# Kernel tuning notes

Measured on AMD Instinct MI355X. Metric: run time of the kernel, lower is better.

## Reference

```python
import jax, jax.numpy as jnp
import numpy as np

L, H, C, V, T_MAX = 12, 12, 768, 50257, 1024
D = C // H
LN_EPS = 1e-5


def layer_norm(x, w, b):
    m = jnp.mean(x, axis=-1, keepdims=True)
    v = jnp.mean(jnp.square(x - m), axis=-1, keepdims=True)
    return (x - m) * jax.lax.rsqrt(v + LN_EPS) * w + b


def setup_inputs() -> dict:
    key = jax.random.key(0)
    ks = jax.random.split(key, 16)
    B, T = 2, 1024
    s = 0.02
    inp = {
        "idx": jax.random.randint(ks[0], (B, T), 0, V),
        "wte": jax.random.normal(ks[1], (V, C), jnp.float32) * s,
        "wpe": jax.random.normal(ks[2], (T_MAX, C), jnp.float32) * s,
        # stacked per-layer params, leading axis = layer
        "ln1_w": jnp.ones((L, C), jnp.float32),
        "ln1_b": jnp.zeros((L, C), jnp.float32),
        "Wq": jax.random.normal(ks[3], (L, C, C), jnp.float32) * s,
        "bq": jnp.zeros((L, C), jnp.float32),
        "Wk": jax.random.normal(ks[4], (L, C, C), jnp.float32) * s,
        "bk": jnp.zeros((L, C), jnp.float32),
        "Wv": jax.random.normal(ks[5], (L, C, C), jnp.float32) * s,
        "bv": jnp.zeros((L, C), jnp.float32),
        "Wo": jax.random.normal(ks[6], (L, C, C), jnp.float32) * (s / np.sqrt(2 * L)),
        "bo": jnp.zeros((L, C), jnp.float32),
        "ln2_w": jnp.ones((L, C), jnp.float32),
        "ln2_b": jnp.zeros((L, C), jnp.float32),
        "Wfc": jax.random.normal(ks[7], (L, C, 4 * C), jnp.float32) * s,
        "bfc": jnp.zeros((L, 4 * C), jnp.float32),
        "Wpr": jax.random.normal(ks[8], (L, 4 * C, C), jnp.float32) * (s / np.sqrt(2 * L)),
        "bpr": jnp.zeros((L, C), jnp.float32),
        "ln_f_w": jnp.ones((C,), jnp.float32),
        "ln_f_b": jnp.zeros((C,), jnp.float32),
        "Wlm": jax.random.normal(ks[9], (C, V), jnp.float32) * s,
    }
    return inp


def _forward(idx, wte, wpe, ln1_w, ln1_b, Wq, bq, Wk, bk, Wv, bv, Wo, bo,
             ln2_w, ln2_b, Wfc, bfc, Wpr, bpr, ln_f_w, ln_f_b, Wlm):
    B, T = idx.shape
    x = wte[idx] + wpe[jnp.arange(T)][None, :, :]  # (B,T,C)
    causal = jnp.tril(jnp.ones((T, T), bool))  # (T,T) causal mask
    scale = 1.0 / np.sqrt(D)
    neg_inf = jnp.finfo(x.dtype).min

    def block(x, p):
        (l1w, l1b, wq, bq_, wk, bk_, wv, bv_, wo, bo_,
         l2w, l2b, wfc, bfc_, wpr, bpr_) = p
        h = layer_norm(x, l1w, l1b)
        q = (h @ wq + bq_).reshape(B, T, H, D)
        k = (h @ wk + bk_).reshape(B, T, H, D)
        v = (h @ wv + bv_).reshape(B, T, H, D)
        scores = jnp.einsum("bqhd,bkhd->bhqk", q, k) * scale
        scores = jnp.where(causal[None, None], scores, neg_inf)
        attn = jax.nn.softmax(scores, axis=-1)
        y = jnp.einsum("bhqk,bkhd->bqhd", attn, v).reshape(B, T, C)
        x = x + y @ wo + bo_
        h2 = layer_norm(x, l2w, l2b)
        x = x + jax.nn.gelu(h2 @ wfc + bfc_, approximate=False) @ wpr + bpr_
        return x, None

    params = (ln1_w, ln1_b, Wq, bq, Wk, bk, Wv, bv, Wo, bo,
              ln2_w, ln2_b, Wfc, bfc, Wpr, bpr)
    x, _ = jax.lax.scan(block, x, params)
    x = layer_norm(x, ln_f_w, ln_f_b)
    logits = x @ Wlm  # (B,T,V)
    return logits


def reference(idx, wte, wpe, ln1_w, ln1_b, Wq, bq, Wk, bk, Wv, bv, Wo, bo,
              ln2_w, ln2_b, Wfc, bfc, Wpr, bpr, ln_f_w, ln_f_b, Wlm):
    return _forward(idx, wte, wpe, ln1_w, ln1_b, Wq, bq, Wk, bk, Wv, bv, Wo, bo,
                    ln2_w, ln2_b, Wfc, bfc, Wpr, bpr, ln_f_w, ln_f_b, Wlm)
```

## Files before the change

### kernel.cpp

```cpp
#include <hip/hip_runtime.h>
#include <math.h>
#include <cstddef>


#define Cdim 768
#define Hn   12
#define Ln   12
#define Tn   1024
#define Bn   2
#define Mrows (Bn * Tn)

typedef unsigned short ushort_t;
typedef __bf16 bf16x8 __attribute__((ext_vector_type(8)));
typedef float  f32x4  __attribute__((ext_vector_type(4)));

__device__ __forceinline__ ushort_t f2bf(float v) {
    union { float f; unsigned int u; } x; x.f = v;
    unsigned int r = x.u + 0x7fffu + ((x.u >> 16) & 1u);
    return (ushort_t)(r >> 16);
}
__device__ __forceinline__ float gelu_f(float v) {
    return 0.5f * v * (1.0f + erff(v * 0.70710678118654752f));
}
__device__ __forceinline__ void gload16(const void* g, void* l) {
    __builtin_amdgcn_global_load_lds(
        (const __attribute__((address_space(1))) unsigned int*)g,
        (__attribute__((address_space(3))) unsigned int*)l, 16, 0, 0);
}

__global__ void embed_k(const int* __restrict__ idx, const float* __restrict__ wte,
                        const float* __restrict__ wpe, float* __restrict__ x) {
    int i = blockIdx.x * 256 + threadIdx.x;
    int c  = i % Cdim;
    int bt = i / Cdim;
    int t  = bt % Tn;
    int tok = idx[bt];
    x[i] = wte[(size_t)tok * Cdim + c] + wpe[(size_t)t * Cdim + c];
}

__global__ __launch_bounds__(256) void ln_k(const float* __restrict__ x,
                                            const float* __restrict__ w,
                                            const float* __restrict__ b,
                                            ushort_t* __restrict__ out) {
    int row = blockIdx.x;
    const float* xr = x + (size_t)row * Cdim;
    int t = threadIdx.x;
    float v0 = xr[t], v1 = xr[t + 256], v2 = xr[t + 512];
    float s = v0 + v1 + v2;
    #pragma unroll
    for (int o = 32; o > 0; o >>= 1) s += __shfl_xor(s, o);
    __shared__ float red[8];
    int wid = t >> 6;
    if ((t & 63) == 0) red[wid] = s;
    __syncthreads();
    float mean = (red[0] + red[1] + red[2] + red[3]) * (1.0f / 768.0f);
    float d0 = v0 - mean, d1 = v1 - mean, d2 = v2 - mean;
    float sq = d0 * d0 + d1 * d1 + d2 * d2;
    #pragma unroll
    for (int o = 32; o > 0; o >>= 1) sq += __shfl_xor(sq, o);
    if ((t & 63) == 0) red[4 + wid] = sq;
    __syncthreads();
    float var = (red[4] + red[5] + red[6] + red[7]) * (1.0f / 768.0f);
    float rstd = rsqrtf(var + 1e-5f);
    ushort_t* orow = out + (size_t)row * Cdim;
    orow[t]       = f2bf(d0 * rstd * w[t]       + b[t]);
    orow[t + 256] = f2bf(d1 * rstd * w[t + 256] + b[t + 256]);
    orow[t + 512] = f2bf(d2 * rstd * w[t + 512] + b[t + 512]);
}

__device__ __forceinline__ void tconv_tile(const float* __restrict__ W,
                                           ushort_t* __restrict__ WT,
                                           int K, int N, int n0, int k0, bool guard) {
    __shared__ float t[32][33];
    int x = threadIdx.x & 31, y = threadIdx.x >> 5;
    #pragma unroll
    for (int j = 0; j < 4; ++j) {
        int kk = k0 + y + j * 8, nn = n0 + x;
        t[y + j * 8][x] = (!guard || nn < N) ? W[(size_t)kk * N + nn] : 0.0f;
    }
    __syncthreads();
    #pragma unroll
    for (int j = 0; j < 4; ++j) {
        int nn = n0 + y + j * 8, kk = k0 + x;
        WT[(size_t)nn * K + kk] = f2bf(t[x][y + j * 8]);
    }
}

__global__ __launch_bounds__(256) void wconv_k(const float* __restrict__ W,
                                               ushort_t* __restrict__ WT,
                                               int K, int N) {
    tconv_tile(W, WT, K, N, blockIdx.x * 32, blockIdx.y * 32, true);
}

__global__ __launch_bounds__(256) void conv_layer_k(
    const float* __restrict__ Wq, const float* __restrict__ Wk,
    const float* __restrict__ Wv, const float* __restrict__ Wo,
    const float* __restrict__ Wfc, const float* __restrict__ Wpr,
    const float* __restrict__ bq, const float* __restrict__ bk,
    const float* __restrict__ bv,
    ushort_t* __restrict__ wqkvt, ushort_t* __restrict__ wot,
    ushort_t* __restrict__ wfct,  ushort_t* __restrict__ wprt,
    float* __restrict__ bqkv) {
    int bid = blockIdx.x;
    if (bid < 2304) {
        int z = bid / 576, t = bid % 576;
        const float* W = (z == 0) ? Wq : (z == 1) ? Wk : (z == 2) ? Wv : Wo;
        ushort_t* dst = (z < 3) ? (wqkvt + (size_t)z * 768 * 768) : wot;
        tconv_tile(W, dst, 768, 768, (t % 24) * 32, (t / 24) * 32, false);
    } else if (bid < 4608) {
        int t = bid - 2304;
        tconv_tile(Wfc, wfct, 768, 3072, (t % 96) * 32, (t / 96) * 32, false);
    } else if (bid < 6912) {
        int t = bid - 4608;
        tconv_tile(Wpr, wprt, 3072, 768, (t % 24) * 32, (t / 24) * 32, false);
    } else {
        int i = (bid - 6912) * 256 + threadIdx.x;
        bqkv[i] = (i < 768) ? bq[i] : (i < 1536 ? bk[i - 768] : bv[i - 1536]);
    }
}

template <int BM, int BN, int TH, int WGN, bool BIAS, bool GELU_, bool OUTBF16, bool XCD>
__global__ __launch_bounds__(TH, 2) void gemm_pipe_k(
    const ushort_t* __restrict__ A,
    const ushort_t* __restrict__ Bt,
    const float* __restrict__ bias,
    void* __restrict__ Cout,
    int M, int N, int K, int cpx, int mtiles) {
    constexpr int SA = BM * 128;
    constexpr int SB = BN * 128;
    constexpr int WM = BM / 2;
    constexpr int WN = BN / WGN;
    constexpr int FM = WM / 16;
    constexpr int FN = WN / 16;
    constexpr int RJ = TH / 8;
    __shared__ char lds[2 * (SA + SB)];
    char* Abase = lds;
    char* Bbase = lds + 2 * SA;

    const int tid = threadIdx.x;
    const int lane = tid & 63;
    const int w = tid >> 6;
    const int wr = w / WGN, wc = w % WGN;
    int m0, n0;
    if (XCD) {
        int lid = ((int)blockIdx.x & 7) * cpx + ((int)blockIdx.x >> 3);
        m0 = (lid % mtiles) * BM;
        n0 = (lid / mtiles) * BN;
    } else {
        m0 = blockIdx.y * BM;
        n0 = blockIdx.x * BN;
    }

    f32x4 acc[FM][FN] = {};

    const int srowl = tid >> 3;
    const int sslot = (tid & 7) ^ (srowl & 7);
    const ushort_t* Asrc = A  + (size_t)(m0 + srowl) * K + sslot * 8;
    const ushort_t* Bsrc = Bt + (size_t)(n0 + srowl) * K + sslot * 8;

    auto stageall = [&](int d, int kt) {
        const ushort_t* As = Asrc + kt * 64;
        const ushort_t* Bs = Bsrc + kt * 64;
        #pragma unroll
        for (int j = 0; j < 4; ++j) {
            gload16(As + (size_t)(j * RJ) * K, Abase + d * SA + tid * 16 + j * (TH * 16));
            gload16(Bs + (size_t)(j * RJ) * K, Bbase + d * SB + tid * 16 + j * (TH * 16));
        }
    };
    auto readA = [&](int d, int m, int ks) -> bf16x8 {
        int rl = wr * WM + m * 16 + (lane & 15);
        int s  = ks * 4 + (lane >> 4);
        return *(const bf16x8*)(Abase + d * SA + rl * 128 + ((s ^ (rl & 7)) << 4));
    };
    auto readB = [&](int d, int n, int ks) -> bf16x8 {
        int rl = wc * WN + n * 16 + (lane & 15);
        int s  = ks * 4 + (lane >> 4);
        return *(const bf16x8*)(Bbase + d * SB + rl * 128 + ((s ^ (rl & 7)) << 4));
    };

    const int nt = K >> 6;
    stageall(0, 0);
    for (int kt = 0; kt < nt; ++kt) {
        const int d = kt & 1;
        if (kt + 1 < nt) {
            stageall(d ^ 1, kt + 1);
            asm volatile("s_waitcnt vmcnt(8)" ::: "memory");
        } else {
            asm volatile("s_waitcnt vmcnt(0)" ::: "memory");
        }
        __builtin_amdgcn_s_barrier();
        asm volatile("" ::: "memory");

        bf16x8 bfr[FN][2];
        #pragma unroll
        for (int n = 0; n < FN; ++n) {
            bfr[n][0] = readB(d, n, 0);
            bfr[n][1] = readB(d, n, 1);
        }
        __builtin_amdgcn_s_setprio(1);
        #pragma unroll
        for (int m = 0; m < FM; ++m) {
            bf16x8 a0 = readA(d, m, 0);
            bf16x8 a1 = readA(d, m, 1);
            #pragma unroll
            for (int n = 0; n < FN; ++n) {
                acc[m][n] = __builtin_amdgcn_mfma_f32_16x16x32_bf16(
                    a0, bfr[n][0], acc[m][n], 0, 0, 0);
                acc[m][n] = __builtin_amdgcn_mfma_f32_16x16x32_bf16(
                    a1, bfr[n][1], acc[m][n], 0, 0, 0);
            }
        }
        __builtin_amdgcn_s_setprio(0);
        asm volatile("" ::: "memory");
        __builtin_amdgcn_s_barrier();
    }

    const int r0 = (lane >> 4) * 4, c0 = lane & 15;
    #pragma unroll
    for (int m = 0; m < FM; ++m)
        #pragma unroll
        for (int n = 0; n < FN; ++n) {
            int col = n0 + wc * WN + n * 16 + c0;
            if (col < N) {
                #pragma unroll
                for (int q = 0; q < 4; ++q) {
                    int row = m0 + wr * WM + m * 16 + r0 + q;
                    float v = acc[m][n][q];
                    if (BIAS) v += bias[col];
                    if (GELU_) v = gelu_f(v);
                    if (OUTBF16) ((ushort_t*)Cout)[(size_t)row * N + col] = f2bf(v);
                    else         ((float*)Cout)[(size_t)row * N + col] = v;
                }
            }
        }
}

template <bool BIAS, bool RES>
__global__ __launch_bounds__(256) void gemm64_k(
    const ushort_t* __restrict__ A, const ushort_t* __restrict__ Bt,
    const float* __restrict__ bias, const float* __restrict__ res,
    float* __restrict__ Cout, int M, int N, int K) {
    __shared__ ushort_t Alds[4][64 * 32];
    __shared__ ushort_t Blds[4][64 * 32];
    const int tid = threadIdx.x;
    const int lane = tid & 63;
    const int w = tid >> 6;
    const int wr = w >> 1, wc = w & 1;
    const int m0 = blockIdx.y * 64;
    const int n0 = blockIdx.x * 64;

    f32x4 acc[2][2] = {};
    const int srow = w * 16 + (lane >> 2);
    const int skoff = (lane & 3) * 8;
    const ushort_t* Ab = A  + (size_t)(m0 + srow) * K + skoff;
    const ushort_t* Bb = Bt + (size_t)(n0 + srow) * K + skoff;

    const int nk = K >> 7;
    for (int kb = 0; kb < nk; ++kb) {
        const int k0 = kb << 7;
        __syncthreads();
        #pragma unroll
        for (int s = 0; s < 4; ++s) {
            gload16(Ab + k0 + s * 32, (char*)&Alds[s][0] + (w * 1024 + lane * 16));
            gload16(Bb + k0 + s * 32, (char*)&Blds[s][0] + (w * 1024 + lane * 16));
        }
        __syncthreads();
        #pragma unroll
        for (int s = 0; s < 4; ++s) {
            bf16x8 af[2], bfr[2];
            #pragma unroll
            for (int i = 0; i < 2; ++i) {
                af[i]  = *(const bf16x8*)((const char*)&Alds[s][0] +
                           ((wr * 32 + i * 16 + (lane & 15)) * 64 + (lane >> 4) * 16));
                bfr[i] = *(const bf16x8*)((const char*)&Blds[s][0] +
                           ((wc * 32 + i * 16 + (lane & 15)) * 64 + (lane >> 4) * 16));
            }
            #pragma unroll
            for (int mi = 0; mi < 2; ++mi)
                #pragma unroll
                for (int ni = 0; ni < 2; ++ni)
                    acc[mi][ni] = __builtin_amdgcn_mfma_f32_16x16x32_bf16(
                        af[mi], bfr[ni], acc[mi][ni], 0, 0, 0);
        }
    }
    const int r0 = (lane >> 4) * 4;
    const int c0 = lane & 15;
    #pragma unroll
    for (int mi = 0; mi < 2; ++mi)
        #pragma unroll
        for (int ni = 0; ni < 2; ++ni) {
            int col = n0 + wc * 32 + ni * 16 + c0;
            #pragma unroll
            for (int q = 0; q < 4; ++q) {
                int row = m0 + wr * 32 + mi * 16 + r0 + q;
                float v = acc[mi][ni][q];
                if (BIAS) v += bias[col];
                if (RES) v += res[(size_t)row * N + col];
                Cout[(size_t)row * N + col] = v;
            }
        }
}

__global__ __launch_bounds__(256) void kvprep_k(const ushort_t* __restrict__ qkvb,
                                                ushort_t* __restrict__ kpb,
                                                ushort_t* __restrict__ vtb) {
    __shared__ ushort_t Ls[256][72];
    const int tc = blockIdx.x, h = blockIdx.y, b = blockIdx.z;
    const int tid = threadIdx.x;
    const int tok = tc * 256 + tid;
    const ushort_t* base = qkvb + (size_t)(b * Tn + tok) * 2304 + h * 64;
    ushort_t* kdst = kpb + ((size_t)(b * Hn + h) * Tn + tok) * 64;
    #pragma unroll
    for (int i = 0; i < 8; ++i)
        *(uint4*)&kdst[i * 8] = *(const uint4*)(base + 768 + i * 8);
    #pragma unroll
    for (int i = 0; i < 8; ++i)
        *(uint4*)&Ls[tid][i * 8] = *(const uint4*)(base + 1536 + i * 8);
    __syncthreads();
    const int d = tid & 63, tg = tid >> 6;
    ushort_t tmp[64];
    #pragma unroll
    for (int i = 0; i < 64; ++i) tmp[i] = Ls[tg * 64 + i][d];
    ushort_t* dst = vtb + ((size_t)(b * Hn + h) * 64 + d) * Tn + tc * 256 + tg * 64;
    #pragma unroll
    for (int i = 0; i < 8; ++i)
        *(uint4*)&dst[i * 8] = *(const uint4*)&tmp[i * 8];
}

__global__ __launch_bounds__(256) void attn_mfma_k(
    const ushort_t* __restrict__ qkvb,
    const ushort_t* __restrict__ kpb,
    const ushort_t* __restrict__ vtb,
    ushort_t* __restrict__ yb) {
    __shared__ ushort_t Ks[64][72];
    __shared__ ushort_t Vt[64][72];
    __shared__ ushort_t Pl[4][16][72];
    const int chunk = (Tn / 64 - 1) - blockIdx.x;
    const int h = blockIdx.y, b = blockIdx.z;
    const int tid = threadIdx.x, lane = tid & 63, w = tid >> 6;
    const int c = lane & 15, g = lane >> 4;
    const int qrow0 = chunk * 64 + w * 16;

    const ushort_t* qp = qkvb + (size_t)(b * Tn + qrow0 + c) * 2304 + h * 64 + g * 8;
    bf16x8 qa0 = *(const bf16x8*)qp;
    bf16x8 qa1 = *(const bf16x8*)(qp + 32);

    f32x4 accO[4] = {};
    float mrun[4], lrun[4];
    #pragma unroll
    for (int q = 0; q < 4; ++q) { mrun[q] = -1e30f; lrun[q] = 0.0f; }

    const int skey = tid >> 2, sd0 = (tid & 3) * 16;
    const ushort_t* ksrc = kpb + ((size_t)(b * Hn + h) * Tn + skey) * 64 + sd0;
    const int vd = tid >> 2, vseg = tid & 3;
    const ushort_t* vsrc = vtb + ((size_t)(b * Hn + h) * 64 + vd) * Tn + vseg * 16;
    ushort_t* KsW = &Ks[skey][sd0];
    ushort_t* VtW = &Vt[vd][vseg * 16];

    const int ntiles = chunk + 1;
    for (int kt = 0; kt < ntiles; ++kt) {
        __syncthreads();
        {
            const ushort_t* kp = ksrc + (size_t)kt * 64 * 64;
            *(uint4*)KsW       = *(const uint4*)kp;
            *(uint4*)(KsW + 8) = *(const uint4*)(kp + 8);
            const ushort_t* vp = vsrc + kt * 64;
            *(uint4*)VtW       = *(const uint4*)vp;
            *(uint4*)(VtW + 8) = *(const uint4*)(vp + 8);
        }
        __syncthreads();

        f32x4 sf[4];
        #pragma unroll
        for (int nk = 0; nk < 4; ++nk) {
            bf16x8 kf0 = *(const bf16x8*)&Ks[nk * 16 + c][g * 8];
            bf16x8 kf1 = *(const bf16x8*)&Ks[nk * 16 + c][g * 8 + 32];
            f32x4 z = {};
            z = __builtin_amdgcn_mfma_f32_16x16x32_bf16(qa0, kf0, z, 0, 0, 0);
            z = __builtin_amdgcn_mfma_f32_16x16x32_bf16(qa1, kf1, z, 0, 0, 0);
            sf[nk] = z;
        }
        float pmax[4] = {-1e30f, -1e30f, -1e30f, -1e30f};
        #pragma unroll
        for (int nk = 0; nk < 4; ++nk) {
            int key = kt * 64 + nk * 16 + c;
            #pragma unroll
            for (int q = 0; q < 4; ++q) {
                float sv = sf[nk][q];
                int row = qrow0 + g * 4 + q;
                sv = (key > row) ? -1e30f : sv;
                sf[nk][q] = sv;
                pmax[q] = fmaxf(pmax[q], sv);
            }
        }
        #pragma unroll
        for (int q = 0; q < 4; ++q)
            #pragma unroll
            for (int off = 1; off < 16; off <<= 1)
                pmax[q] = fmaxf(pmax[q], __shfl_xor(pmax[q], off));
        float corr[4], psum[4];
        #pragma unroll
        for (int q = 0; q < 4; ++q) {
            float mn = fmaxf(mrun[q], pmax[q]);
            corr[q] = __expf((mrun[q] - mn) * 0.125f);
            mrun[q] = mn;
            psum[q] = 0.0f;
        }
        #pragma unroll
        for (int nk = 0; nk < 4; ++nk)
            #pragma unroll
            for (int q = 0; q < 4; ++q) {
                float p = __expf((sf[nk][q] - mrun[q]) * 0.125f);
                psum[q] += p;
                Pl[w][g * 4 + q][nk * 16 + c] = f2bf(p);
            }
        #pragma unroll
        for (int q = 0; q < 4; ++q) {
            #pragma unroll
            for (int off = 1; off < 16; off <<= 1)
                psum[q] += __shfl_xor(psum[q], off);
            lrun[q] = lrun[q] * corr[q] + psum[q];
        }
        #pragma unroll
        for (int ni = 0; ni < 4; ++ni)
            #pragma unroll
            for (int q = 0; q < 4; ++q)
                accO[ni][q] *= corr[q];

        asm volatile("" ::: "memory");
        bf16x8 pa0 = *(const bf16x8*)&Pl[w][c][g * 8];
        bf16x8 pa1 = *(const bf16x8*)&Pl[w][c][g * 8 + 32];
        #pragma unroll
        for (int ni = 0; ni < 4; ++ni) {
            bf16x8 bv0 = *(const bf16x8*)&Vt[ni * 16 + c][g * 8];
            bf16x8 bv1 = *(const bf16x8*)&Vt[ni * 16 + c][g * 8 + 32];
            accO[ni] = __builtin_amdgcn_mfma_f32_16x16x32_bf16(pa0, bv0, accO[ni], 0, 0, 0);
            accO[ni] = __builtin_amdgcn_mfma_f32_16x16x32_bf16(pa1, bv1, accO[ni], 0, 0, 0);
        }
    }

    #pragma unroll
    for (int q = 0; q < 4; ++q) {
        float inv = 1.0f / lrun[q];
        ushort_t* yr = yb + (size_t)(b * Tn + qrow0 + g * 4 + q) * Cdim + h * 64;
        #pragma unroll
        for (int ni = 0; ni < 4; ++ni)
            yr[ni * 16 + c] = f2bf(accO[ni][q] * inv);
    }
}

extern "C" void kernel_launch(void* const* d_in, const int* in_sizes, int n_in,
                              void* d_out, int out_size, void* d_ws, size_t ws_size,
                              hipStream_t stream) {
    const int*   idx  = (const int*)d_in[0];
    const float* wte  = (const float*)d_in[1];
    const float* wpe  = (const float*)d_in[2];
    const float* ln1w = (const float*)d_in[3];
    const float* ln1b = (const float*)d_in[4];
    const float* Wq   = (const float*)d_in[5];
    const float* bq   = (const float*)d_in[6];
    const float* Wk   = (const float*)d_in[7];
    const float* bk   = (const float*)d_in[8];
    const float* Wv   = (const float*)d_in[9];
    const float* bv   = (const float*)d_in[10];
    const float* Wo   = (const float*)d_in[11];
    const float* bo   = (const float*)d_in[12];
    const float* ln2w = (const float*)d_in[13];
    const float* ln2b = (const float*)d_in[14];
    const float* Wfc  = (const float*)d_in[15];
    const float* bfc  = (const float*)d_in[16];
    const float* Wpr  = (const float*)d_in[17];
    const float* bpr  = (const float*)d_in[18];
    const float* lnfw = (const float*)d_in[19];
    const float* lnfb = (const float*)d_in[20];
    const float* Wlm  = (const float*)d_in[21];
    float* out = (float*)d_out;

    const int M = Mrows;
    const int V = out_size / M;
    const int Vpad = ((V + 255) / 256) * 256;

    float*    x     = (float*)d_ws;
    float*    bqkv  = x + (size_t)M * Cdim;
    ushort_t* qkvb  = (ushort_t*)(bqkv + 2304);
    ushort_t* kpb   = qkvb + (size_t)M * 2304;
    ushort_t* vtb   = kpb + (size_t)Bn * Hn * Tn * 64;
    ushort_t* hb    = vtb + (size_t)Bn * Hn * 64 * Tn;
    ushort_t* yb    = hb + (size_t)M * Cdim;
    ushort_t* mid   = yb + (size_t)M * Cdim;
    ushort_t* wqkvt = mid + (size_t)M * 3072;
    ushort_t* wot   = wqkvt + (size_t)2304 * Cdim;
    ushort_t* wfct  = wot + (size_t)Cdim * Cdim;
    ushort_t* wprt  = wfct + (size_t)3072 * Cdim;
    ushort_t* wlmt  = wprt + (size_t)Cdim * 3072;

    embed_k<<<(M * Cdim) / 256, 256, 0, stream>>>(idx, wte, wpe, x);

    for (int l = 0; l < Ln; ++l) {
        const size_t wo2 = (size_t)l * Cdim * Cdim;
        const size_t wo4 = (size_t)l * Cdim * 4 * Cdim;
        conv_layer_k<<<6921, 256, 0, stream>>>(
            Wq + wo2, Wk + wo2, Wv + wo2, Wo + wo2, Wfc + wo4, Wpr + wo4,
            bq + l * Cdim, bk + l * Cdim, bv + l * Cdim,
            wqkvt, wot, wfct, wprt, bqkv);

        ln_k<<<M, 256, 0, stream>>>(x, ln1w + l * Cdim, ln1b + l * Cdim, hb);
        gemm_pipe_k<128, 128, 256, 2, true, false, true, false>
            <<<dim3(18, 16), 256, 0, stream>>>(
            hb, wqkvt, bqkv, qkvb, M, 2304, Cdim, 0, 0);
        kvprep_k<<<dim3(4, Hn, Bn), 256, 0, stream>>>(qkvb, kpb, vtb);
        attn_mfma_k<<<dim3(16, Hn, Bn), 256, 0, stream>>>(qkvb, kpb, vtb, yb);
        gemm64_k<true, true><<<dim3(12, 32), 256, 0, stream>>>(
            yb, wot, bo + l * Cdim, x, x, M, Cdim, Cdim);
        ln_k<<<M, 256, 0, stream>>>(x, ln2w + l * Cdim, ln2b + l * Cdim, hb);
        gemm_pipe_k<128, 128, 256, 2, true, true, true, false>
            <<<dim3(24, 16), 256, 0, stream>>>(
            hb, wfct, bfc + (size_t)l * 4 * Cdim, mid, M, 3072, Cdim, 0, 0);
        gemm64_k<true, true><<<dim3(12, 32), 256, 0, stream>>>(
            mid, wprt, bpr + l * Cdim, x, x, M, Cdim, 3072);
    }

    ln_k<<<M, 256, 0, stream>>>(x, lnfw, lnfb, hb);
    wconv_k<<<dim3(Vpad / 32, 24), 256, 0, stream>>>(Wlm, wlmt, Cdim, V);
    const int nblk = (Vpad / 256) * 8;
    gemm_pipe_k<256, 256, 512, 4, false, false, false, true>
        <<<nblk, 512, 0, stream>>>(
        hb, wlmt, nullptr, out, M, V, Cdim, nblk / 8, 8);
}
```

Before: 2.045 ms.

## Use pipelined GEMM with residual epilogue for out-proj/FC2 and smaller LM-head tiles

Generalizes the double-buffered pipelined GEMM to support a residual-add epilogue and configurable per-tile load counts, then uses it (64x64 tiles) in place of the simple synchronous gemm64 kernel for the attention output and MLP projection GEMMs. The LM-head GEMM switches from 256x256 tiles with 512 threads to 128x128 tiles with 256 threads and XCD remapping, giving more blocks. The aim is to overlap global loads with MFMA in the skinny N=768 GEMMs and to improve occupancy and load balance for the vocab projection. The smaller LM-head tiles reduce data reuse per block.

```diff
diff --git a/kernel.cpp b/kernel.cpp
--- a/kernel.cpp
+++ b/kernel.cpp
@@ -119,11 +119,13 @@
     }
 }
 
-template <int BM, int BN, int TH, int WGN, bool BIAS, bool GELU_, bool OUTBF16, bool XCD>
+template <int BM, int BN, int TH, int WGN,
+          bool BIAS, bool GELU_, bool RES, bool OUTBF16, bool XCD>
 __global__ __launch_bounds__(TH, 2) void gemm_pipe_k(
     const ushort_t* __restrict__ A,
     const ushort_t* __restrict__ Bt,
     const float* __restrict__ bias,
+    const float* __restrict__ res,
     void* __restrict__ Cout,
     int M, int N, int K, int cpx, int mtiles) {
     constexpr int SA = BM * 128;
@@ -133,6 +135,10 @@
     constexpr int FM = WM / 16;
     constexpr int FN = WN / 16;
     constexpr int RJ = TH / 8;
+    constexpr int JA = BM / RJ;
+    constexpr int JB = BN / RJ;
+    constexpr int NL = JA + JB;
+    static_assert(NL == 4 || NL == 8, "vmcnt immediate");
     __shared__ char lds[2 * (SA + SB)];
     char* Abase = lds;
     char* Bbase = lds + 2 * SA;
@@ -162,10 +168,11 @@
         const ushort_t* As = Asrc + kt * 64;
         const ushort_t* Bs = Bsrc + kt * 64;
         #pragma unroll
-        for (int j = 0; j < 4; ++j) {
+        for (int j = 0; j < JA; ++j)
             gload16(As + (size_t)(j * RJ) * K, Abase + d * SA + tid * 16 + j * (TH * 16));
+        #pragma unroll
+        for (int j = 0; j < JB; ++j)
             gload16(Bs + (size_t)(j * RJ) * K, Bbase + d * SB + tid * 16 + j * (TH * 16));
-        }
     };
     auto readA = [&](int d, int m, int ks) -> bf16x8 {
         int rl = wr * WM + m * 16 + (lane & 15);
@@ -184,7 +191,8 @@
         const int d = kt & 1;
         if (kt + 1 < nt) {
             stageall(d ^ 1, kt + 1);
-            asm volatile("s_waitcnt vmcnt(8)" ::: "memory");
+            if constexpr (NL == 8) asm volatile("s_waitcnt vmcnt(8)" ::: "memory");
+            else                   asm volatile("s_waitcnt vmcnt(4)" ::: "memory");
         } else {
             asm volatile("s_waitcnt vmcnt(0)" ::: "memory");
         }
@@ -228,75 +236,10 @@
                     float v = acc[m][n][q];
                     if (BIAS) v += bias[col];
                     if (GELU_) v = gelu_f(v);
+                    if (RES) v += res[(size_t)row * N + col];
                     if (OUTBF16) ((ushort_t*)Cout)[(size_t)row * N + col] = f2bf(v);
                     else         ((float*)Cout)[(size_t)row * N + col] = v;
                 }
-            }
-        }
-}
-
-template <bool BIAS, bool RES>
-__global__ __launch_bounds__(256) void gemm64_k(
-    const ushort_t* __restrict__ A, const ushort_t* __restrict__ Bt,
-    const float* __restrict__ bias, const float* __restrict__ res,
-    float* __restrict__ Cout, int M, int N, int K) {
-    __shared__ ushort_t Alds[4][64 * 32];
-    __shared__ ushort_t Blds[4][64 * 32];
-    const int tid = threadIdx.x;
-    const int lane = tid & 63;
-    const int w = tid >> 6;
-    const int wr = w >> 1, wc = w & 1;
-    const int m0 = blockIdx.y * 64;
-    const int n0 = blockIdx.x * 64;
-
-    f32x4 acc[2][2] = {};
-    const int srow = w * 16 + (lane >> 2);
-    const int skoff = (lane & 3) * 8;
-    const ushort_t* Ab = A  + (size_t)(m0 + srow) * K + skoff;
-    const ushort_t* Bb = Bt + (size_t)(n0 + srow) * K + skoff;
-
-    const int nk = K >> 7;
-    for (int kb = 0; kb < nk; ++kb) {
-        const int k0 = kb << 7;
-        __syncthreads();
-        #pragma unroll
-        for (int s = 0; s < 4; ++s) {
-            gload16(Ab + k0 + s * 32, (char*)&Alds[s][0] + (w * 1024 + lane * 16));
-            gload16(Bb + k0 + s * 32, (char*)&Blds[s][0] + (w * 1024 + lane * 16));
-        }
-        __syncthreads();
-        #pragma unroll
-        for (int s = 0; s < 4; ++s) {
-            bf16x8 af[2], bfr[2];
-            #pragma unroll
-            for (int i = 0; i < 2; ++i) {
-                af[i]  = *(const bf16x8*)((const char*)&Alds[s][0] +
-                           ((wr * 32 + i * 16 + (lane & 15)) * 64 + (lane >> 4) * 16));
-                bfr[i] = *(const bf16x8*)((const char*)&Blds[s][0] +
-                           ((wc * 32 + i * 16 + (lane & 15)) * 64 + (lane >> 4) * 16));
-            }
-            #pragma unroll
-            for (int mi = 0; mi < 2; ++mi)
-                #pragma unroll
-                for (int ni = 0; ni < 2; ++ni)
-                    acc[mi][ni] = __builtin_amdgcn_mfma_f32_16x16x32_bf16(
-                        af[mi], bfr[ni], acc[mi][ni], 0, 0, 0);
-        }
-    }
-    const int r0 = (lane >> 4) * 4;
-    const int c0 = lane & 15;
-    #pragma unroll
-    for (int mi = 0; mi < 2; ++mi)
-        #pragma unroll
-        for (int ni = 0; ni < 2; ++ni) {
-            int col = n0 + wc * 32 + ni * 16 + c0;
-            #pragma unroll
-            for (int q = 0; q < 4; ++q) {
-                int row = m0 + wr * 32 + mi * 16 + r0 + q;
-                float v = acc[mi][ni][q];
-                if (BIAS) v += bias[col];
-                if (RES) v += res[(size_t)row * N + col];
-                Cout[(size_t)row * N + col] = v;
             }
         }
 }
@@ -505,25 +448,27 @@
             wqkvt, wot, wfct, wprt, bqkv);
 
         ln_k<<<M, 256, 0, stream>>>(x, ln1w + l * Cdim, ln1b + l * Cdim, hb);
-        gemm_pipe_k<128, 128, 256, 2, true, false, true, false>
+        gemm_pipe_k<128, 128, 256, 2, true, false, false, true, false>
             <<<dim3(18, 16), 256, 0, stream>>>(
-            hb, wqkvt, bqkv, qkvb, M, 2304, Cdim, 0, 0);
+            hb, wqkvt, bqkv, nullptr, qkvb, M, 2304, Cdim, 0, 0);
         kvprep_k<<<dim3(4, Hn, Bn), 256, 0, stream>>>(qkvb, kpb, vtb);
         attn_mfma_k<<<dim3(16, Hn, Bn), 256, 0, stream>>>(qkvb, kpb, vtb, yb);
-        gemm64_k<true, true><<<dim3(12, 32), 256, 0, stream>>>(
-            yb, wot, bo + l * Cdim, x, x, M, Cdim, Cdim);
+        gemm_pipe_k<64, 64, 256, 2, true, false, true, false, false>
+            <<<dim3(12, 32), 256, 0, stream>>>(
+            yb, wot, bo + l * Cdim, x, x, M, Cdim, Cdim, 0, 0);
         ln_k<<<M, 256, 0, stream>>>(x, ln2w + l * Cdim, ln2b + l * Cdim, hb);
-        gemm_pipe_k<128, 128, 256, 2, true, true, true, false>
+        gemm_pipe_k<128, 128, 256, 2, true, true, false, true, false>
             <<<dim3(24, 16), 256, 0, stream>>>(
-            hb, wfct, bfc + (size_t)l * 4 * Cdim, mid, M, 3072, Cdim, 0, 0);
-        gemm64_k<true, true><<<dim3(12, 32), 256, 0, stream>>>(
-            mid, wprt, bpr + l * Cdim, x, x, M, Cdim, 3072);
+            hb, wfct, bfc + (size_t)l * 4 * Cdim, nullptr, mid, M, 3072, Cdim, 0, 0);
+        gemm_pipe_k<64, 64, 256, 2, true, false, true, false, false>
+            <<<dim3(12, 32), 256, 0, stream>>>(
+            mid, wprt, bpr + l * Cdim, x, x, M, Cdim, 3072, 0, 0);
     }
 
     ln_k<<<M, 256, 0, stream>>>(x, lnfw, lnfb, hb);
     wconv_k<<<dim3(Vpad / 32, 24), 256, 0, stream>>>(Wlm, wlmt, Cdim, V);
-    const int nblk = (Vpad / 256) * 8;
-    gemm_pipe_k<256, 256, 512, 4, false, false, false, true>
-        <<<nblk, 512, 0, stream>>>(
-        hb, wlmt, nullptr, out, M, V, Cdim, nblk / 8, 8);
-}
+    const int nblk = 16 * (Vpad / 128);
+    gemm_pipe_k<128, 128, 256, 2, false, false, false, false, true>
+        <<<nblk, 256, 0, stream>>>(
+        hb, wlmt, nullptr, nullptr, out, M, V, Cdim, nblk / 8, 16);
+}
```

New measurement: 1.971 ms. 1.04x faster.
